# Kernel optimization log

Measured on AMD Instinct MI355X. Metric: run time of the kernel, lower is better.

The kernel has to match this reference:

```python
import jax, jax.numpy as jnp
import numpy as np

D = 1024   # visual_dim
N = 64     # num_phrases(1) * topN(64)
DEG = 16   # edges per subject row (incl. one guaranteed via a permutation)
E = N * DEG
T = 2      # cfg.MODEL.RELATION.VISUAL_GRAPH_PASSING_TIME


def _graph():
    rng = np.random.default_rng(0)
    perm = rng.permutation(N)
    mask = np.zeros((N, N), bool)
    for i in range(N):
        mask[i, perm[i]] = True  # permutation guarantees every column is covered
        pool = np.delete(np.arange(N), perm[i])
        mask[i, rng.choice(pool, DEG - 1, replace=False)] = True
    hdim, wdim = np.nonzero(mask)  # row-major, exactly E entries
    conn = np.full((N, N), -1, np.int32)
    conn[hdim, wdim] = np.arange(hdim.shape[0])
    edge_idx = hdim * N + wdim  # original: hdim*topN + wdim (topN == N since num_phrases == 1)
    return conn, edge_idx.astype(np.int32)


def setup_inputs():
    conn, edge_idx = _graph()
    key = jax.random.key(0)
    ks = jax.random.split(key, 16)
    p = lambda k, shp: jax.random.normal(k, shp, jnp.float32) * 0.02
    return {
        'visual_feat': jax.random.normal(ks[0], (N, D), jnp.float32),
        'rel_visual_feat': jax.random.normal(ks[1], (E, D), jnp.float32),
        'conn_map': jnp.asarray(conn),
        'topN_boxes_ids': jnp.arange(N, dtype=jnp.int32)[None, :],  # only shape is used
        'edge_idx': jnp.asarray(edge_idx),
        'W_sub': p(ks[2], (D, D)),
        'W_obj': p(ks[3], (D, D)),
        'W_r2s': p(ks[4], (D, D)),
        'W_r2o': p(ks[5], (D, D)),
        'W_joint': p(ks[6], (D, 4 * D)),
        'W_ctx': p(ks[7], (D, 3 * D)),
        'W_rel_update': p(ks[8], (D, 3 * D)),
        'W_rel_joint': p(ks[9], (D, 4 * D)),
        'W_rel_ctx': p(ks[10], (D, 2 * D)),
        'W_node': p(ks[11], (D, 2 * D)),
        'b_node': jnp.zeros((D,), jnp.float32),
        'W_factor': p(ks[12], (D, 2 * D)),
    }


def _forward(visual_feat, rel_visual_feat, conn_map, edge_idx,
             W_sub, W_obj, W_r2s, W_r2o, W_joint, W_ctx, W_rel_update,
             W_rel_joint, W_rel_ctx, W_node, b_node, W_factor):
    n, d = visual_feat.shape
    scale = jnp.asarray(d, visual_feat.dtype) ** 0.5
    connected = conn_map >= 0
    # scatter edge features into the dense [N, N, D] grid
    rel_temp = (jnp.zeros((n * n, d), visual_feat.dtype)
                .at[edge_idx].set(rel_visual_feat)
                .reshape(n, n, d))
    rel_ctx = rel_temp
    vctx = visual_feat
    for _ in range(T):
        # joint node embedding  [N, D]
        vj = jnp.concatenate([visual_feat, vctx, visual_feat * vctx, vctx - visual_feat], 1) @ W_joint.T
        # joint edge embedding  [N, N, D] (1x1 conv == per-position linear)
        rj = jnp.einsum('ijd,od->ijo',
                        jnp.concatenate([rel_temp, rel_ctx, rel_temp * rel_ctx, rel_temp - rel_ctx], 2),
                        W_rel_joint)
        # node -> edge: cat(sub_tile, obj_tile, rj) @ W_rel_update, done without tiling
        Ws, Wo, Wr = W_rel_update[:, :d], W_rel_update[:, d:2 * d], W_rel_update[:, 2 * d:]
        rel_j = (vj @ Ws.T)[:, None, :] + (vj @ Wo.T)[None, :, :] + jnp.einsum('ijd,od->ijo', rj, Wr)
        # edge -> node attention scores (elementwise product of 1x1-conv outputs, summed over channels)
        s_sbj = jnp.einsum('id,ijd->ij', vj @ W_sub.T, jnp.einsum('ijd,od->ijo', rel_j, W_r2s)) / scale
        s_obj = jnp.einsum('jd,ijd->ij', vj @ W_obj.T, jnp.einsum('ijd,od->ijo', rel_j, W_r2o)) / scale
        w_sbj = jax.nn.softmax(jnp.where(connected, s_sbj, -jnp.inf), axis=1)
        w_obj = jax.nn.softmax(jnp.where(connected, s_obj, -jnp.inf), axis=0)
        ctx = jnp.concatenate([jnp.einsum('ijd,ij->id', rel_j, w_sbj),
                               jnp.einsum('ijd,ij->jd', rel_j, w_obj)], 1)
        vctx = jnp.concatenate([vctx, ctx], 1) @ W_ctx.T
        rel_ctx = jnp.einsum('ijd,od->ijo', jnp.concatenate([rel_ctx, rel_j], 2), W_rel_ctx)
    # gather back the valid edges and produce outputs
    rel_out = jnp.concatenate([rel_visual_feat, rel_ctx.reshape(-1, d)[edge_idx]], 1) @ W_factor.T
    v_out = jnp.concatenate([visual_feat, vctx], 1) @ W_node.T + b_node
    deg = connected.sum(1) + connected.sum(0)
    v_out = jnp.where((deg == 0)[:, None], visual_feat, v_out)  # isolated nodes pass through
    return rel_out, v_out


def reference(visual_feat, rel_visual_feat, conn_map, topN_boxes_ids, edge_idx,
              W_sub, W_obj, W_r2s, W_r2o, W_joint, W_ctx, W_rel_update,
              W_rel_joint, W_rel_ctx, W_node, b_node, W_factor):
    del topN_boxes_ids  # only its shape is used in the original
    return _forward(visual_feat, rel_visual_feat, conn_map, edge_idx,
                    W_sub, W_obj, W_r2s, W_r2o, W_joint, W_ctx, W_rel_update,
                    W_rel_joint, W_rel_ctx, W_node, b_node, W_factor)
```

## Files before the change

kernel.cpp:

```cpp
#include <hip/hip_runtime.h>

static constexpr int kN = 64;
static constexpr int kD = 1024;
static constexpr int kE = 1024;
static constexpr int kT = 2;

typedef short  bf16x8 __attribute__((ext_vector_type(8)));
typedef float  f32x4  __attribute__((ext_vector_type(4)));
typedef unsigned short us8 __attribute__((ext_vector_type(8)));
typedef unsigned short us4 __attribute__((ext_vector_type(4)));

__device__ __forceinline__ unsigned short f2b(float f) {
    unsigned int u = __builtin_bit_cast(unsigned int, f);
    u += 0x7FFFu + ((u >> 16) & 1u);
    return (unsigned short)(u >> 16);
}
__device__ __forceinline__ float b2f(unsigned short u) {
    unsigned int x = ((unsigned int)u) << 16;
    return __builtin_bit_cast(float, x);
}
__device__ __forceinline__ bf16x8 cvt8(float4 a, float4 b) {
    us8 o;
    o[0] = f2b(a.x); o[1] = f2b(a.y); o[2] = f2b(a.z); o[3] = f2b(a.w);
    o[4] = f2b(b.x); o[5] = f2b(b.y); o[6] = f2b(b.z); o[7] = f2b(b.w);
    return __builtin_bit_cast(bf16x8, o);
}

struct ASrc { const unsigned short* s0; const unsigned short* s1; const unsigned short* s2; int mode; };

__device__ __forceinline__ bf16x8 loadA8(const ASrc& s, int row, int kg) {
    const int seg = kg >> 10, k = kg & 1023;
    const size_t ro = (size_t)row * 1024 + k;
    if (s.mode == 1) {
        const unsigned short* p = (seg == 0) ? s.s0 : (seg == 1 ? s.s1 : s.s2);
        return *(const bf16x8*)(p + ro);
    }
    const bf16x8 a = *(const bf16x8*)(s.s0 + ro);
    if (seg == 0) return a;
    const bf16x8 b = *(const bf16x8*)(s.s1 + ro);
    const us8 ua = __builtin_bit_cast(us8, a), ub = __builtin_bit_cast(us8, b);
    us8 o;
#pragma unroll
    for (int q = 0; q < 8; ++q) o[q] = f2b(b2f(ua[q]) * b2f(ub[q]));
    return __builtin_bit_cast(bf16x8, o);
}

struct GJob { ASrc a; const unsigned short* W; int ldw; void* P; int M; int K; int KS; int pbf; };
struct GJobs { GJob j[5]; int t0[6]; int nj; };

__global__ __launch_bounds__(256)
void k_gemm(GJobs G)
{
    __shared__ unsigned short lds[12288];
    const int flat = blockIdx.x;
    int ji = 0;
    while (ji + 1 < G.nj && flat >= G.t0[ji + 1]) ++ji;
    const GJob J = G.j[ji];
    const int local = flat - G.t0[ji];
    const int rowTiles = J.M >> 6;
    const int rt = local & (rowTiles - 1);
    const int rest = local / rowTiles;
    const int ct = rest & 7, z = rest >> 3;
    const int rowBase = rt * 64, colBase = ct * 128;
    const int kchunk = J.K / J.KS, kbeg = z * kchunk, kend = kbeg + kchunk;

    const int tid = threadIdx.x, lane = tid & 63, wid = tid >> 6;
    const int sr = tid >> 3, sc8 = tid & 7;
    const int wc8 = (sc8 ^ (sr & 7)) * 8;

    bf16x8 ra[2], rb[4];
    auto stage = [&](int kt) {
#pragma unroll
        for (int h = 0; h < 2; ++h)
            ra[h] = loadA8(J.a, rowBase + sr + 32 * h, kt + sc8 * 8);
#pragma unroll
        for (int h = 0; h < 4; ++h)
            rb[h] = *(const bf16x8*)(J.W + (size_t)(colBase + sr + 32 * h) * J.ldw + kt + sc8 * 8);
    };

    f32x4 acc[2][4] = {};
    const int wr = wid >> 1, wc = wid & 1;
    const int l15 = lane & 15, l4 = lane >> 4;

    stage(kbeg);
    for (int kt = kbeg; kt < kend; kt += 64) {
        __syncthreads();
#pragma unroll
        for (int h = 0; h < 2; ++h)
            *(bf16x8*)&lds[(sr + 32 * h) * 64 + wc8] = ra[h];
#pragma unroll
        for (int h = 0; h < 4; ++h)
            *(bf16x8*)&lds[4096 + (sr + 32 * h) * 64 + wc8] = rb[h];
        __syncthreads();
        if (kt + 64 < kend) stage(kt + 64);
#pragma unroll
        for (int kk = 0; kk < 2; ++kk) {
            const int c8 = kk * 4 + l4;
            bf16x8 af[2], bv[4];
#pragma unroll
            for (int m = 0; m < 2; ++m) {
                const int ar = wr * 32 + m * 16 + l15;
                af[m] = *(const bf16x8*)&lds[ar * 64 + (c8 ^ (ar & 7)) * 8];
            }
#pragma unroll
            for (int n = 0; n < 4; ++n) {
                const int br = wc * 64 + n * 16 + l15;
                bv[n] = *(const bf16x8*)&lds[4096 + br * 64 + (c8 ^ (br & 7)) * 8];
            }
#pragma unroll
            for (int m = 0; m < 2; ++m)
#pragma unroll
                for (int n = 0; n < 4; ++n)
                    acc[m][n] = __builtin_amdgcn_mfma_f32_16x16x32_bf16(af[m], bv[n], acc[m][n], 0, 0, 0);
        }
    }

    if (J.pbf) {
        __syncthreads();
#pragma unroll
        for (int m = 0; m < 2; ++m)
#pragma unroll
            for (int n = 0; n < 4; ++n)
#pragma unroll
                for (int r = 0; r < 4; ++r)
                    lds[(wr * 32 + m * 16 + l4 * 4 + r) * 132 + wc * 64 + n * 16 + l15] =
                        f2b(acc[m][n][r]);
        __syncthreads();
        unsigned short* Pb = (unsigned short*)J.P + (size_t)z * J.M * 1024;
#pragma unroll
        for (int c = tid; c < 1024; c += 256) {
            const int row = c >> 4, ch = c & 15;
            *(bf16x8*)(Pb + (size_t)(rowBase + row) * 1024 + colBase + ch * 8) =
                *(const bf16x8*)&lds[row * 132 + ch * 8];
        }
    } else {
        float* base = (float*)J.P + (size_t)z * J.M * 1024;
#pragma unroll
        for (int m = 0; m < 2; ++m) {
            const int row = rowBase + wr * 32 + m * 16 + l4 * 4;
#pragma unroll
            for (int n = 0; n < 4; ++n) {
                const int col = colBase + wc * 64 + n * 16 + l15;
#pragma unroll
                for (int r = 0; r < 4; ++r)
                    base[(size_t)(row + r) * 1024 + col] = acc[m][n][r];
            }
        }
    }
}

struct RJob { const void* P; int MO8; int KS; int pbf; float* Cf; unsigned short* Cb;
              const unsigned short* addb; const float* bias; int gather; };
struct RJobs { RJob j[6]; int t0[7]; int nj; const int* eidx; const float* gP; int gKS; };

__global__ void k_reduce(RJobs R)
{
    const int flat = blockIdx.x;
    int ji = 0;
    while (ji + 1 < R.nj && flat >= R.t0[ji + 1]) ++ji;
    const RJob J = R.j[ji];
    const int i8 = (flat - R.t0[ji]) * 256 + threadIdx.x;
    if (i8 >= J.MO8) return;
    float s[8] = {0.f, 0.f, 0.f, 0.f, 0.f, 0.f, 0.f, 0.f};
    if (J.pbf) {
        const unsigned short* P = (const unsigned short*)J.P;
        for (int z = 0; z < J.KS; ++z) {
            const us8 v = *(const us8*)(P + (size_t)z * J.MO8 * 8 + (size_t)i8 * 8);
#pragma unroll
            for (int q = 0; q < 8; ++q) s[q] += b2f(v[q]);
        }
    } else {
        const float* P = (const float*)J.P;
        for (int z = 0; z < J.KS; ++z) {
            const float* p = P + (size_t)z * J.MO8 * 8 + (size_t)i8 * 8;
            const float4 v0 = *(const float4*)p;
            const float4 v1 = *(const float4*)(p + 4);
            s[0] += v0.x; s[1] += v0.y; s[2] += v0.z; s[3] += v0.w;
            s[4] += v1.x; s[5] += v1.y; s[6] += v1.z; s[7] += v1.w;
        }
    }
    if (J.addb) {
        const us8 v = *(const us8*)(J.addb + (size_t)i8 * 8);
#pragma unroll
        for (int q = 0; q < 8; ++q) s[q] += b2f(v[q]);
    }
    if (J.gather) {
        const int e = i8 >> 7, c8 = i8 & 127;
        const int idx = R.eidx[e];
        const float* as_ = R.gP + (size_t)(idx >> 6) * 1024 + c8 * 8;
        const float* ao_ = R.gP + 131072 + (size_t)(idx & 63) * 1024 + c8 * 8;
        for (int z = 0; z < R.gKS; ++z) {
#pragma unroll
            for (int q = 0; q < 8; ++q)
                s[q] += as_[(size_t)z * 65536 + q] + ao_[(size_t)z * 65536 + q];
        }
    }
    if (J.bias) {
        const int c8 = i8 & 127;
#pragma unroll
        for (int q = 0; q < 8; ++q) s[q] += J.bias[c8 * 8 + q];
    }
    if (J.Cf) {
        *(float4*)(J.Cf + (size_t)i8 * 8)     = make_float4(s[0], s[1], s[2], s[3]);
        *(float4*)(J.Cf + (size_t)i8 * 8 + 4) = make_float4(s[4], s[5], s[6], s[7]);
    }
    if (J.Cb) {
        us8 o;
#pragma unroll
        for (int q = 0; q < 8; ++q) o[q] = f2b(s[q]);
        *(us8*)(J.Cb + (size_t)i8 * 8) = o;
    }
}

struct ConvBatch { const float* s[7]; unsigned short* d[7]; int beg8[7]; int total8; };
__global__ void k_f2b_batch(ConvBatch cb)
{
    int i = blockIdx.x * blockDim.x + threadIdx.x;
    if (i >= cb.total8) return;
    int k = 0;
    while (k < 6 && i >= cb.beg8[k + 1]) ++k;
    const int j = i - cb.beg8[k];
    const float4 v0 = reinterpret_cast<const float4*>(cb.s[k])[2 * j];
    const float4 v1 = reinterpret_cast<const float4*>(cb.s[k])[2 * j + 1];
    const bf16x8 o = cvt8(v0, v1);
    *(bf16x8*)(cb.d[k] + (size_t)j * 8) = o;
}

struct T4 { const float* s[4]; unsigned short* d[4]; };
__global__ __launch_bounds__(256)
void k_transpose(T4 t4)
{
    __shared__ float tile[64][65];
    const float* __restrict__ src = t4.s[blockIdx.z];
    unsigned short* __restrict__ dst = t4.d[blockIdx.z];
    const int bx = blockIdx.x * 64, by = blockIdx.y * 64;
    const int c = threadIdx.x & 63, r0 = threadIdx.x >> 6;
#pragma unroll
    for (int h = 0; h < 16; ++h) {
        const int r = r0 * 16 + h;
        tile[r][c] = src[(size_t)(by + r) * 1024 + bx + c];
    }
    __syncthreads();
#pragma unroll
    for (int h = 0; h < 16; ++h) {
        const int kk = r0 * 16 + h;
        dst[(size_t)(bx + kk) * 1024 + by + c] = f2b(tile[c][kk]);
    }
}

__global__ __launch_bounds__(256)
void k_buildW(const float* __restrict__ Wrel, const float* __restrict__ Wjnt,
              unsigned short* __restrict__ WrtRel, unsigned short* __restrict__ WeffRel,
              unsigned short* __restrict__ UrtVj, unsigned short* __restrict__ UeffVj)
{
    const int idx = blockIdx.x * 256 + threadIdx.x;
    const int o = idx >> 8, j = (idx & 255) * 4;
    const float* W = blockIdx.z ? Wjnt : Wrel;
    const float sgn = blockIdx.z ? -1.f : 1.f;
    unsigned short* rt = blockIdx.z ? UrtVj : WrtRel;
    unsigned short* ef = blockIdx.z ? UeffVj : WeffRel;
    const float4 w1 = *(const float4*)(W + (size_t)o * 4096 + j);
    const float4 w2 = *(const float4*)(W + (size_t)o * 4096 + 1024 + j);
    const float4 w3 = *(const float4*)(W + (size_t)o * 4096 + 2048 + j);
    const float4 w4 = *(const float4*)(W + (size_t)o * 4096 + 3072 + j);
    us4 t;
    t.x = f2b(w1.x + sgn * w4.x); t.y = f2b(w1.y + sgn * w4.y);
    t.z = f2b(w1.z + sgn * w4.z); t.w = f2b(w1.w + sgn * w4.w);
    *(us4*)(rt + (size_t)o * 1024 + j) = t;
    t.x = f2b(w2.x - sgn * w4.x); t.y = f2b(w2.y - sgn * w4.y);
    t.z = f2b(w2.z - sgn * w4.z); t.w = f2b(w2.w - sgn * w4.w);
    *(us4*)(ef + (size_t)o * 2048 + j) = t;
    t.x = f2b(w3.x); t.y = f2b(w3.y); t.z = f2b(w3.z); t.w = f2b(w3.w);
    *(us4*)(ef + (size_t)o * 2048 + 1024 + j) = t;
}

__global__ __launch_bounds__(256)
void k_scores(const float* __restrict__ qws, const float* __restrict__ qwo,
              const float* __restrict__ relj, const int* __restrict__ eidx,
              float* __restrict__ s_sbj, float* __restrict__ s_obj)
{
    const int e = blockIdx.x, t = threadIdx.x;
    const int idx = eidx[e];
    const int i = idx >> 6, j = idx & 63;
    const float4 r = reinterpret_cast<const float4*>(relj)[(size_t)e * 256 + t];
    const float4 a = reinterpret_cast<const float4*>(qws)[(size_t)i * 256 + t];
    const float4 b = reinterpret_cast<const float4*>(qwo)[(size_t)j * 256 + t];
    float vs = a.x * r.x + a.y * r.y + a.z * r.z + a.w * r.w;
    float vo = b.x * r.x + b.y * r.y + b.z * r.z + b.w * r.w;
    for (int off = 32; off; off >>= 1) {
        vs += __shfl_down(vs, off);
        vo += __shfl_down(vo, off);
    }
    __shared__ float ss[4], so[4];
    const int w = t >> 6, lane = t & 63;
    if (lane == 0) { ss[w] = vs; so[w] = vo; }
    __syncthreads();
    if (t == 0) {
        s_sbj[e] = (ss[0] + ss[1] + ss[2] + ss[3]) * 0.03125f;
        s_obj[e] = (so[0] + so[1] + so[2] + so[3]) * 0.03125f;
    }
}

__global__ __launch_bounds__(256)
void k_ctx12(const float* __restrict__ relj, const float* __restrict__ s_sbj,
             const float* __restrict__ s_obj, const int* __restrict__ conn,
             unsigned short* __restrict__ ctx1b, unsigned short* __restrict__ ctx2b)
{
    const int bid = blockIdx.x, t = threadIdx.x;
    const float4* relj4 = reinterpret_cast<const float4*>(relj);
    float4 acc = make_float4(0.f, 0.f, 0.f, 0.f);
    if (bid < 64) {
        const int i = bid;
        float sv[16];
        float m = -1e30f;
#pragma unroll
        for (int q = 0; q < 16; ++q) { sv[q] = s_sbj[i * 16 + q]; m = fmaxf(m, sv[q]); }
        float sum = 0.f;
#pragma unroll
        for (int q = 0; q < 16; ++q) { sv[q] = expf(sv[q] - m); sum += sv[q]; }
        const float inv = 1.f / sum;
#pragma unroll
        for (int q = 0; q < 16; ++q) {
            const float w = sv[q] * inv;
            const float4 v = relj4[(size_t)(i * 16 + q) * 256 + t];
            acc.x += w * v.x; acc.y += w * v.y; acc.z += w * v.z; acc.w += w * v.w;
        }
        us4 o; o.x = f2b(acc.x); o.y = f2b(acc.y); o.z = f2b(acc.z); o.w = f2b(acc.w);
        *(us4*)(ctx1b + (size_t)bid * 1024 + t * 4) = o;
    } else {
        const int j = bid - 64;
        __shared__ float sl[64];
        __shared__ int el[64];
        if (t < 64) {
            const int e = conn[t * kN + j];
            el[t] = e;
            sl[t] = (e >= 0) ? s_obj[e] : -1e30f;
        }
        __syncthreads();
        float m = -1e30f;
        for (int i = 0; i < 64; ++i) m = fmaxf(m, sl[i]);
        __syncthreads();
        if (t < 64) sl[t] = (el[t] >= 0) ? expf(sl[t] - m) : 0.f;
        __syncthreads();
        float sum = 0.f;
        for (int i = 0; i < 64; ++i) sum += sl[i];
        const float inv = 1.f / sum;
        for (int i = 0; i < 64; ++i) {
            const int e = el[i];
            if (e >= 0) {
                const float w = sl[i] * inv;
                const float4 v = relj4[(size_t)e * 256 + t];
                acc.x += w * v.x; acc.y += w * v.y; acc.z += w * v.z; acc.w += w * v.w;
            }
        }
        us4 o; o.x = f2b(acc.x); o.y = f2b(acc.y); o.z = f2b(acc.z); o.w = f2b(acc.w);
        *(us4*)(ctx2b + (size_t)j * 1024 + t * 4) = o;
    }
}

extern "C" void kernel_launch(void* const* d_in, const int* in_sizes, int n_in,
                              void* d_out, int out_size, void* d_ws, size_t ws_size,
                              hipStream_t stream)
{
    const float* visual   = (const float*)d_in[0];
    const float* relvis   = (const float*)d_in[1];
    const int*   conn     = (const int*)d_in[2];
    const int*   edge_idx = (const int*)d_in[4];
    const float* W_sub    = (const float*)d_in[5];
    const float* W_obj    = (const float*)d_in[6];
    const float* W_r2s    = (const float*)d_in[7];
    const float* W_r2o    = (const float*)d_in[8];
    const float* W_joint  = (const float*)d_in[9];
    const float* W_ctx    = (const float*)d_in[10];
    const float* W_relu   = (const float*)d_in[11];
    const float* W_relj   = (const float*)d_in[12];
    const float* W_relc   = (const float*)d_in[13];
    const float* W_node   = (const float*)d_in[14];
    const float* b_node   = (const float*)d_in[15];
    const float* W_factor = (const float*)d_in[16];
    (void)in_sizes; (void)n_in; (void)out_size; (void)ws_size;

    float* ws = (float*)d_ws;
    size_t off = 0;
    auto allocF = [&](size_t n) { float* p = ws + off; off += n; return p; };
    auto allocU = [&](size_t n) { return (unsigned short*)allocF((n + 1) / 2); };

    float* partF = allocF((size_t)1024 * 1024);
    unsigned short* partB = allocU((size_t)16 * 1024 * 1024);
    float* asqw  = allocF((size_t)4 * 64 * 1024);
    float* relj  = allocF((size_t)kE * kD);
    float* s_sbj = allocF(kE);
    float* s_obj = allocF(kE);
    unsigned short* relvis_b = allocU((size_t)kE * kD);
    unsigned short* visual_b = allocU((size_t)kN * kD);
    unsigned short* vj_b   = allocU((size_t)kN * kD);
    unsigned short* rj_b   = allocU((size_t)kE * kD);
    unsigned short* relj_b = allocU((size_t)kE * kD);
    unsigned short* rc_bA  = allocU((size_t)kE * kD);
    unsigned short* rc_bB  = allocU((size_t)kE * kD);
    unsigned short* vctx_bA = allocU((size_t)kN * kD);
    unsigned short* vctx_bB = allocU((size_t)kN * kD);
    unsigned short* ctx1_b = allocU((size_t)kN * kD);
    unsigned short* ctx2_b = allocU((size_t)kN * kD);
    unsigned short* R0_b = allocU((size_t)kE * kD);
    unsigned short* G0_b = allocU((size_t)kN * kD);
    unsigned short* Wb_ctx    = allocU((size_t)kD * 3 * kD);
    unsigned short* Wb_relu   = allocU((size_t)kD * 3 * kD);
    unsigned short* Wb_relc   = allocU((size_t)kD * 2 * kD);
    unsigned short* Wb_node   = allocU((size_t)kD * 2 * kD);
    unsigned short* Wb_factor = allocU((size_t)kD * 2 * kD);
    unsigned short* WsubT = allocU((size_t)kD * kD);
    unsigned short* WobjT = allocU((size_t)kD * kD);
    unsigned short* Wr2sT = allocU((size_t)kD * kD);
    unsigned short* Wr2oT = allocU((size_t)kD * kD);
    unsigned short* Wc_s  = allocU((size_t)kD * kD);
    unsigned short* Wc_o  = allocU((size_t)kD * kD);
    unsigned short* WrtRel  = allocU((size_t)kD * kD);
    unsigned short* WeffRel = allocU((size_t)kD * 2 * kD);
    unsigned short* UrtVj   = allocU((size_t)kD * kD);
    unsigned short* UeffVj  = allocU((size_t)kD * 2 * kD);

    auto seg1 = [](const unsigned short* a) {
        ASrc s; s.s0 = a; s.s1 = nullptr; s.s2 = nullptr; s.mode = 1; return s;
    };
    auto seg2 = [](const unsigned short* a, const unsigned short* b) {
        ASrc s; s.s0 = a; s.s1 = b; s.s2 = nullptr; s.mode = 1; return s;
    };
    auto seg3 = [](const unsigned short* a, const unsigned short* b, const unsigned short* c) {
        ASrc s; s.s0 = a; s.s1 = b; s.s2 = c; s.mode = 1; return s;
    };
    auto prodA = [](const unsigned short* c, const unsigned short* x) {
        ASrc s; s.s0 = c; s.s1 = x; s.s2 = nullptr; s.mode = 2; return s;
    };

    GJobs G; RJobs R;
    int gn = 0, gt = 0, rn = 0, rtt = 0;
    auto gAdd = [&](ASrc a, const unsigned short* W, int ldw, void* P, int M, int K, int KS, int pbf) {
        G.j[gn].a = a; G.j[gn].W = W; G.j[gn].ldw = ldw; G.j[gn].P = P;
        G.j[gn].M = M; G.j[gn].K = K; G.j[gn].KS = KS; G.j[gn].pbf = pbf;
        G.t0[gn] = gt; gt += KS * (M >> 6) * 8; ++gn;
    };
    auto gLaunch = [&]() {
        G.nj = gn; G.t0[gn] = gt;
        hipLaunchKernelGGL(k_gemm, dim3(gt), dim3(256), 0, stream, G);
        gn = 0; gt = 0;
    };
    auto rAdd = [&](const void* P, int MO8, int KS, int pbf, float* Cf, unsigned short* Cb,
                    const unsigned short* addb, const float* bias, int gather) {
        R.j[rn].P = P; R.j[rn].MO8 = MO8; R.j[rn].KS = KS; R.j[rn].pbf = pbf;
        R.j[rn].Cf = Cf; R.j[rn].Cb = Cb; R.j[rn].addb = addb; R.j[rn].bias = bias;
        R.j[rn].gather = gather;
        R.t0[rn] = rtt; rtt += (MO8 + 255) / 256; ++rn;
    };
    auto rLaunch = [&](const int* eidx, const float* gP, int gKS) {
        R.nj = rn; R.t0[rn] = rtt; R.eidx = eidx; R.gP = gP; R.gKS = gKS;
        hipLaunchKernelGGL(k_reduce, dim3(rtt), dim3(256), 0, stream, R);
        rn = 0; rtt = 0;
    };

    {
        ConvBatch cb;
        const float* srcs[7] = {W_ctx, W_relu, W_relc, W_node, W_factor, relvis, visual};
        unsigned short* dsts[7] = {Wb_ctx, Wb_relu, Wb_relc, Wb_node, Wb_factor, relvis_b, visual_b};
        const int nel[7] = {3 * 1024 * 1024, 3 * 1024 * 1024, 2 * 1024 * 1024,
                            2 * 1024 * 1024, 2 * 1024 * 1024, 1024 * 1024, 64 * 1024};
        int cum = 0;
        for (int k = 0; k < 7; ++k) { cb.s[k] = srcs[k]; cb.d[k] = dsts[k]; cb.beg8[k] = cum; cum += nel[k] / 8; }
        cb.total8 = cum;
        hipLaunchKernelGGL(k_f2b_batch, dim3((cum + 255) / 256), dim3(256), 0, stream, cb);
    }
    {
        T4 t4;
        t4.s[0] = W_sub; t4.d[0] = WsubT;
        t4.s[1] = W_obj; t4.d[1] = WobjT;
        t4.s[2] = W_r2s; t4.d[2] = Wr2sT;
        t4.s[3] = W_r2o; t4.d[3] = Wr2oT;
        hipLaunchKernelGGL(k_transpose, dim3(16, 16, 4), dim3(256), 0, stream, t4);
    }
    hipLaunchKernelGGL(k_buildW, dim3(1024, 1, 2), dim3(256), 0, stream,
                       W_relj, W_joint, WrtRel, WeffRel, UrtVj, UeffVj);

    const size_t PB1 = (size_t)4 * 1024 * 1024;
    gAdd(seg1(Wr2sT), WsubT, 1024, partB, 1024, 1024, 4, 1);
    gAdd(seg1(Wr2oT), WobjT, 1024, partB + PB1, 1024, 1024, 4, 1);
    gAdd(seg1(relvis_b), WrtRel, 1024, partB + 2 * PB1, 1024, 1024, 4, 1);
    gAdd(seg1(visual_b), UrtVj, 1024, partF, 64, 1024, 4, 0);
    gLaunch();
    rAdd(partB, 131072, 4, 1, nullptr, Wc_s, nullptr, nullptr, 0);
    rAdd(partB + PB1, 131072, 4, 1, nullptr, Wc_o, nullptr, nullptr, 0);
    rAdd(partB + 2 * PB1, 131072, 4, 1, nullptr, R0_b, nullptr, nullptr, 0);
    rAdd(partF, 8192, 4, 0, nullptr, G0_b, nullptr, nullptr, 0);
    rLaunch(nullptr, nullptr, 0);

    for (int t = 0; t < kT; ++t) {
        const unsigned short* vcur  = (t == 0) ? visual_b : vctx_bA;
        unsigned short*       vnext = (t == 0) ? vctx_bA : vctx_bB;
        const unsigned short* rccur = (t == 0) ? relvis_b : rc_bA;
        unsigned short*       rcnext = (t == 0) ? rc_bA : rc_bB;

        gAdd(prodA(vcur, visual_b), UeffVj, 2048, partF, 64, 2048, 8, 0);
        gAdd(prodA(rccur, relvis_b), WeffRel, 2048, partB, 1024, 2048, 8, 1);
        gLaunch();
        rAdd(partF, 8192, 8, 0, nullptr, vj_b, G0_b, nullptr, 0);
        rAdd(partB, 131072, 8, 1, nullptr, rj_b, R0_b, nullptr, 0);
        rLaunch(nullptr, nullptr, 0);

        gAdd(seg1(vj_b), Wb_relu,        3072, partF,          64, 1024, 2, 0);
        gAdd(seg1(vj_b), Wb_relu + 1024, 3072, partF + 131072, 64, 1024, 2, 0);
        gAdd(seg1(vj_b), Wc_s,           1024, partF + 262144, 64, 1024, 2, 0);
        gAdd(seg1(vj_b), Wc_o,           1024, partF + 393216, 64, 1024, 2, 0);
        gAdd(seg1(rj_b), Wb_relu + 2048, 3072, partB,        1024, 1024, 4, 1);
        gLaunch();
        rAdd(partF,          8192, 2, 0, asqw,          nullptr, nullptr, nullptr, 0);
        rAdd(partF + 131072, 8192, 2, 0, asqw + 65536,  nullptr, nullptr, nullptr, 0);
        rAdd(partF + 262144, 8192, 2, 0, asqw + 131072, nullptr, nullptr, nullptr, 0);
        rAdd(partF + 393216, 8192, 2, 0, asqw + 196608, nullptr, nullptr, nullptr, 0);
        rAdd(partB, 131072, 4, 1, relj, relj_b, nullptr, nullptr, 1);
        rLaunch(edge_idx, partF, 2);

        hipLaunchKernelGGL(k_scores, dim3(kE), dim3(256), 0, stream,
                           asqw + 131072, asqw + 196608, relj, edge_idx, s_sbj, s_obj);
        hipLaunchKernelGGL(k_ctx12, dim3(128), dim3(256), 0, stream,
                           relj, s_sbj, s_obj, conn, ctx1_b, ctx2_b);

        gAdd(seg3(vcur, ctx1_b, ctx2_b), Wb_ctx, 3072, partF, 64, 3072, 8, 0);
        gAdd(seg2(rccur, relj_b), Wb_relc, 2048, partB, 1024, 2048, 8, 1);
        gLaunch();
        rAdd(partF, 8192, 8, 0, nullptr, vnext, nullptr, nullptr, 0);
        rAdd(partB, 131072, 8, 1, nullptr, rcnext, nullptr, nullptr, 0);
        rLaunch(nullptr, nullptr, 0);
    }

    float* rel_out = (float*)d_out;
    float* v_out   = (float*)d_out + (size_t)kE * kD;
    gAdd(seg2(relvis_b, rc_bB), Wb_factor, 2048, partB, 1024, 2048, 4, 1);
    gAdd(seg2(visual_b, vctx_bB), Wb_node, 2048, partF, 64, 2048, 8, 0);
    gLaunch();
    rAdd(partB, 131072, 4, 1, rel_out, nullptr, nullptr, nullptr, 0);
    rAdd(partF, 8192, 8, 0, v_out, nullptr, nullptr, b_node, 0);
    rLaunch(nullptr, nullptr, 0);
}
```

Baseline: 222.4 us.

## Use 128-row GEMM tiles with register-resident B and fuse score into context kernel

For large-M GEMM jobs the kernel now uses 128x128 tiles and a 4x4 MFMA accumulator per wave. B fragments are loaded straight from global memory into registers with double buffering, and only A is staged through LDS. This cuts LDS traffic and the block count, and raises per-wave compute density, at the cost of higher register pressure and fewer blocks for parallelism. Separately, the per-edge score kernel is folded into the context softmax kernel, which computes the dot products itself and removes one launch plus the score round-trip through global memory.

```diff
diff --git a/kernel.cpp b/kernel.cpp
--- a/kernel.cpp
+++ b/kernel.cpp
@@ -51,93 +51,153 @@
 __global__ __launch_bounds__(256)
 void k_gemm(GJobs G)
 {
-    __shared__ unsigned short lds[12288];
+    __shared__ unsigned short lds[16896];
     const int flat = blockIdx.x;
     int ji = 0;
     while (ji + 1 < G.nj && flat >= G.t0[ji + 1]) ++ji;
     const GJob J = G.j[ji];
     const int local = flat - G.t0[ji];
-    const int rowTiles = J.M >> 6;
-    const int rt = local & (rowTiles - 1);
-    const int rest = local / rowTiles;
-    const int ct = rest & 7, z = rest >> 3;
-    const int rowBase = rt * 64, colBase = ct * 128;
-    const int kchunk = J.K / J.KS, kbeg = z * kchunk, kend = kbeg + kchunk;
-
     const int tid = threadIdx.x, lane = tid & 63, wid = tid >> 6;
+    const int l15 = lane & 15, l4 = lane >> 4;
     const int sr = tid >> 3, sc8 = tid & 7;
     const int wc8 = (sc8 ^ (sr & 7)) * 8;
 
-    bf16x8 ra[2], rb[4];
-    auto stage = [&](int kt) {
-#pragma unroll
-        for (int h = 0; h < 2; ++h)
-            ra[h] = loadA8(J.a, rowBase + sr + 32 * h, kt + sc8 * 8);
-#pragma unroll
-        for (int h = 0; h < 4; ++h)
-            rb[h] = *(const bf16x8*)(J.W + (size_t)(colBase + sr + 32 * h) * J.ldw + kt + sc8 * 8);
-    };
-
-    f32x4 acc[2][4] = {};
-    const int wr = wid >> 1, wc = wid & 1;
-    const int l15 = lane & 15, l4 = lane >> 4;
-
-    stage(kbeg);
-    for (int kt = kbeg; kt < kend; kt += 64) {
+    if (J.M >= 128) {
+        const int rowTiles = J.M >> 7;
+        const int rt = local % rowTiles;
+        const int rest = local / rowTiles;
+        const int ct = rest & 7, z = rest >> 3;
+        const int rowBase = rt * 128, colBase = ct * 128;
+        const int kchunk = J.K / J.KS, kbeg = z * kchunk, kend = kbeg + kchunk;
+        const int wr = wid >> 1, wc = wid & 1;
+
+        f32x4 acc[4][4] = {};
+        bf16x8 ra[4], rb0[8], rb1[8];
+        const unsigned short* Bbase =
+            J.W + (size_t)(colBase + wc * 64 + l15) * J.ldw + l4 * 8;
+
+        auto stageA = [&](int kt) {
+#pragma unroll
+            for (int h = 0; h < 4; ++h)
+                ra[h] = loadA8(J.a, rowBase + sr + 32 * h, kt + sc8 * 8);
+        };
+        auto loadB = [&](int kt, bf16x8* rb) {
+#pragma unroll
+            for (int n = 0; n < 4; ++n) {
+                rb[n]     = *(const bf16x8*)(Bbase + (size_t)(n * 16) * J.ldw + kt);
+                rb[4 + n] = *(const bf16x8*)(Bbase + (size_t)(n * 16) * J.ldw + kt + 32);
+            }
+        };
+        auto writeA = [&]() {
+#pragma unroll
+            for (int h = 0; h < 4; ++h)
+                *(bf16x8*)&lds[(sr + 32 * h) * 64 + wc8] = ra[h];
+        };
+        auto compute = [&](bf16x8* rb) {
+#pragma unroll
+            for (int kk = 0; kk < 2; ++kk) {
+                bf16x8 af[4];
+#pragma unroll
+                for (int m = 0; m < 4; ++m) {
+                    const int ar = wr * 64 + m * 16 + l15;
+                    af[m] = *(const bf16x8*)&lds[ar * 64 + (((kk << 2) | l4) ^ (ar & 7)) * 8];
+                }
+#pragma unroll
+                for (int m = 0; m < 4; ++m)
+#pragma unroll
+                    for (int n = 0; n < 4; ++n)
+                        acc[m][n] = __builtin_amdgcn_mfma_f32_16x16x32_bf16(
+                            af[m], rb[kk * 4 + n], acc[m][n], 0, 0, 0);
+            }
+        };
+
+        stageA(kbeg); loadB(kbeg, rb0);
+        for (int kt = kbeg; kt < kend; kt += 128) {
+            __syncthreads();
+            writeA();
+            __syncthreads();
+            const bool more1 = (kt + 64 < kend);
+            if (more1) { stageA(kt + 64); loadB(kt + 64, rb1); }
+            compute(rb0);
+            if (!more1) break;
+            __syncthreads();
+            writeA();
+            __syncthreads();
+            const bool more2 = (kt + 128 < kend);
+            if (more2) { stageA(kt + 128); loadB(kt + 128, rb0); }
+            compute(rb1);
+        }
+
         __syncthreads();
 #pragma unroll
-        for (int h = 0; h < 2; ++h)
-            *(bf16x8*)&lds[(sr + 32 * h) * 64 + wc8] = ra[h];
-#pragma unroll
-        for (int h = 0; h < 4; ++h)
-            *(bf16x8*)&lds[4096 + (sr + 32 * h) * 64 + wc8] = rb[h];
-        __syncthreads();
-        if (kt + 64 < kend) stage(kt + 64);
-#pragma unroll
-        for (int kk = 0; kk < 2; ++kk) {
-            const int c8 = kk * 4 + l4;
-            bf16x8 af[2], bv[4];
-#pragma unroll
-            for (int m = 0; m < 2; ++m) {
-                const int ar = wr * 32 + m * 16 + l15;
-                af[m] = *(const bf16x8*)&lds[ar * 64 + (c8 ^ (ar & 7)) * 8];
-            }
-#pragma unroll
-            for (int n = 0; n < 4; ++n) {
-                const int br = wc * 64 + n * 16 + l15;
-                bv[n] = *(const bf16x8*)&lds[4096 + br * 64 + (c8 ^ (br & 7)) * 8];
-            }
-#pragma unroll
-            for (int m = 0; m < 2; ++m)
-#pragma unroll
-                for (int n = 0; n < 4; ++n)
-                    acc[m][n] = __builtin_amdgcn_mfma_f32_16x16x32_bf16(af[m], bv[n], acc[m][n], 0, 0, 0);
-        }
-    }
-
-    if (J.pbf) {
-        __syncthreads();
-#pragma unroll
-        for (int m = 0; m < 2; ++m)
+        for (int m = 0; m < 4; ++m)
 #pragma unroll
             for (int n = 0; n < 4; ++n)
 #pragma unroll
                 for (int r = 0; r < 4; ++r)
-                    lds[(wr * 32 + m * 16 + l4 * 4 + r) * 132 + wc * 64 + n * 16 + l15] =
+                    lds[(wr * 64 + m * 16 + l4 * 4 + r) * 132 + wc * 64 + n * 16 + l15] =
                         f2b(acc[m][n][r]);
         __syncthreads();
         unsigned short* Pb = (unsigned short*)J.P + (size_t)z * J.M * 1024;
 #pragma unroll
-        for (int c = tid; c < 1024; c += 256) {
+        for (int c = tid; c < 2048; c += 256) {
             const int row = c >> 4, ch = c & 15;
             *(bf16x8*)(Pb + (size_t)(rowBase + row) * 1024 + colBase + ch * 8) =
                 *(const bf16x8*)&lds[row * 132 + ch * 8];
         }
     } else {
+        const int ct = local & 7, z = local >> 3;
+        const int colBase = ct * 128;
+        const int kchunk = J.K / J.KS, kbeg = z * kchunk, kend = kbeg + kchunk;
+        const int wr = wid >> 1, wc = wid & 1;
+
+        bf16x8 ra[2], rb[4];
+        auto stage = [&](int kt) {
+#pragma unroll
+            for (int h = 0; h < 2; ++h)
+                ra[h] = loadA8(J.a, sr + 32 * h, kt + sc8 * 8);
+#pragma unroll
+            for (int h = 0; h < 4; ++h)
+                rb[h] = *(const bf16x8*)(J.W + (size_t)(colBase + sr + 32 * h) * J.ldw + kt + sc8 * 8);
+        };
+
+        f32x4 acc[2][4] = {};
+        stage(kbeg);
+        for (int kt = kbeg; kt < kend; kt += 64) {
+            __syncthreads();
+#pragma unroll
+            for (int h = 0; h < 2; ++h)
+                *(bf16x8*)&lds[(sr + 32 * h) * 64 + wc8] = ra[h];
+#pragma unroll
+            for (int h = 0; h < 4; ++h)
+                *(bf16x8*)&lds[4096 + (sr + 32 * h) * 64 + wc8] = rb[h];
+            __syncthreads();
+            if (kt + 64 < kend) stage(kt + 64);
+#pragma unroll
+            for (int kk = 0; kk < 2; ++kk) {
+                const int c8 = kk * 4 + l4;
+                bf16x8 af[2], bv[4];
+#pragma unroll
+                for (int m = 0; m < 2; ++m) {
+                    const int ar = wr * 32 + m * 16 + l15;
+                    af[m] = *(const bf16x8*)&lds[ar * 64 + (c8 ^ (ar & 7)) * 8];
+                }
+#pragma unroll
+                for (int n = 0; n < 4; ++n) {
+                    const int br = wc * 64 + n * 16 + l15;
+                    bv[n] = *(const bf16x8*)&lds[4096 + br * 64 + (c8 ^ (br & 7)) * 8];
+                }
+#pragma unroll
+                for (int m = 0; m < 2; ++m)
+#pragma unroll
+                    for (int n = 0; n < 4; ++n)
+                        acc[m][n] = __builtin_amdgcn_mfma_f32_16x16x32_bf16(af[m], bv[n], acc[m][n], 0, 0, 0);
+            }
+        }
         float* base = (float*)J.P + (size_t)z * J.M * 1024;
 #pragma unroll
         for (int m = 0; m < 2; ++m) {
-            const int row = rowBase + wr * 32 + m * 16 + l4 * 4;
+            const int row = wr * 32 + m * 16 + l4 * 4;
 #pragma unroll
             for (int n = 0; n < 4; ++n) {
                 const int col = colBase + wc * 64 + n * 16 + l15;
@@ -275,46 +335,40 @@
 }
 
 __global__ __launch_bounds__(256)
-void k_scores(const float* __restrict__ qws, const float* __restrict__ qwo,
-              const float* __restrict__ relj, const int* __restrict__ eidx,
-              float* __restrict__ s_sbj, float* __restrict__ s_obj)
-{
-    const int e = blockIdx.x, t = threadIdx.x;
-    const int idx = eidx[e];
-    const int i = idx >> 6, j = idx & 63;
-    const float4 r = reinterpret_cast<const float4*>(relj)[(size_t)e * 256 + t];
-    const float4 a = reinterpret_cast<const float4*>(qws)[(size_t)i * 256 + t];
-    const float4 b = reinterpret_cast<const float4*>(qwo)[(size_t)j * 256 + t];
-    float vs = a.x * r.x + a.y * r.y + a.z * r.z + a.w * r.w;
-    float vo = b.x * r.x + b.y * r.y + b.z * r.z + b.w * r.w;
-    for (int off = 32; off; off >>= 1) {
-        vs += __shfl_down(vs, off);
-        vo += __shfl_down(vo, off);
-    }
-    __shared__ float ss[4], so[4];
-    const int w = t >> 6, lane = t & 63;
-    if (lane == 0) { ss[w] = vs; so[w] = vo; }
-    __syncthreads();
-    if (t == 0) {
-        s_sbj[e] = (ss[0] + ss[1] + ss[2] + ss[3]) * 0.03125f;
-        s_obj[e] = (so[0] + so[1] + so[2] + so[3]) * 0.03125f;
-    }
-}
-
-__global__ __launch_bounds__(256)
-void k_ctx12(const float* __restrict__ relj, const float* __restrict__ s_sbj,
-             const float* __restrict__ s_obj, const int* __restrict__ conn,
-             unsigned short* __restrict__ ctx1b, unsigned short* __restrict__ ctx2b)
+void k_sctx(const float* __restrict__ relj, const float* __restrict__ qws,
+            const float* __restrict__ qwo, const int* __restrict__ conn,
+            unsigned short* __restrict__ ctx1b, unsigned short* __restrict__ ctx2b)
 {
     const int bid = blockIdx.x, t = threadIdx.x;
     const float4* relj4 = reinterpret_cast<const float4*>(relj);
+    __shared__ float sl[64];
+    __shared__ int el[64];
     float4 acc = make_float4(0.f, 0.f, 0.f, 0.f);
+
     if (bid < 64) {
         const int i = bid;
+        {
+            const int g = t >> 4, l = t & 15;
+            const size_t e4 = (size_t)(i * 16 + g) * 256;
+            const float4* q4 = reinterpret_cast<const float4*>(qws) + (size_t)i * 256;
+            float v = 0.f;
+#pragma unroll
+            for (int q = 0; q < 16; ++q) {
+                const float4 r = relj4[e4 + l + q * 16];
+                const float4 a = q4[l + q * 16];
+                v += a.x * r.x + a.y * r.y + a.z * r.z + a.w * r.w;
+            }
+            v += __shfl_xor(v, 1, 16);
+            v += __shfl_xor(v, 2, 16);
+            v += __shfl_xor(v, 4, 16);
+            v += __shfl_xor(v, 8, 16);
+            if (l == 0) sl[g] = v * 0.03125f;
+        }
+        __syncthreads();
         float sv[16];
         float m = -1e30f;
 #pragma unroll
-        for (int q = 0; q < 16; ++q) { sv[q] = s_sbj[i * 16 + q]; m = fmaxf(m, sv[q]); }
+        for (int q = 0; q < 16; ++q) { sv[q] = sl[q]; m = fmaxf(m, sv[q]); }
         float sum = 0.f;
 #pragma unroll
         for (int q = 0; q < 16; ++q) { sv[q] = expf(sv[q] - m); sum += sv[q]; }
@@ -326,29 +380,42 @@
             acc.x += w * v.x; acc.y += w * v.y; acc.z += w * v.z; acc.w += w * v.w;
         }
         us4 o; o.x = f2b(acc.x); o.y = f2b(acc.y); o.z = f2b(acc.z); o.w = f2b(acc.w);
-        *(us4*)(ctx1b + (size_t)bid * 1024 + t * 4) = o;
+        *(us4*)(ctx1b + (size_t)i * 1024 + t * 4) = o;
     } else {
         const int j = bid - 64;
-        __shared__ float sl[64];
-        __shared__ int el[64];
-        if (t < 64) {
-            const int e = conn[t * kN + j];
-            el[t] = e;
-            sl[t] = (e >= 0) ? s_obj[e] : -1e30f;
+        {
+            const int i = t >> 2, sub = t & 3;
+            const int e = conn[i * kN + j];
+            if (sub == 0) el[i] = e;
+            float v = 0.f;
+            if (e >= 0) {
+                const size_t e4 = (size_t)e * 256;
+                const float4* q4 = reinterpret_cast<const float4*>(qwo) + (size_t)j * 256;
+#pragma unroll
+                for (int q = 0; q < 64; ++q) {
+                    const float4 r = relj4[e4 + sub + q * 4];
+                    const float4 a = q4[sub + q * 4];
+                    v += a.x * r.x + a.y * r.y + a.z * r.z + a.w * r.w;
+                }
+            }
+            v += __shfl_xor(v, 1, 4);
+            v += __shfl_xor(v, 2, 4);
+            if (sub == 0) sl[i] = (e >= 0) ? v * 0.03125f : -1e30f;
         }
         __syncthreads();
         float m = -1e30f;
         for (int i = 0; i < 64; ++i) m = fmaxf(m, sl[i]);
-        __syncthreads();
-        if (t < 64) sl[t] = (el[t] >= 0) ? expf(sl[t] - m) : 0.f;
-        __syncthreads();
         float sum = 0.f;
-        for (int i = 0; i < 64; ++i) sum += sl[i];
+        float ex[64];
+        for (int i = 0; i < 64; ++i) {
+            ex[i] = (el[i] >= 0) ? expf(sl[i] - m) : 0.f;
+            sum += ex[i];
+        }
         const float inv = 1.f / sum;
         for (int i = 0; i < 64; ++i) {
             const int e = el[i];
             if (e >= 0) {
-                const float w = sl[i] * inv;
+                const float w = ex[i] * inv;
                 const float4 v = relj4[(size_t)e * 256 + t];
                 acc.x += w * v.x; acc.y += w * v.y; acc.z += w * v.z; acc.w += w * v.w;
             }
@@ -389,8 +456,6 @@
     unsigned short* partB = allocU((size_t)16 * 1024 * 1024);
     float* asqw  = allocF((size_t)4 * 64 * 1024);
     float* relj  = allocF((size_t)kE * kD);
-    float* s_sbj = allocF(kE);
-    float* s_obj = allocF(kE);
     unsigned short* relvis_b = allocU((size_t)kE * kD);
     unsigned short* visual_b = allocU((size_t)kN * kD);
     unsigned short* vj_b   = allocU((size_t)kN * kD);
@@ -438,7 +503,9 @@
     auto gAdd = [&](ASrc a, const unsigned short* W, int ldw, void* P, int M, int K, int KS, int pbf) {
         G.j[gn].a = a; G.j[gn].W = W; G.j[gn].ldw = ldw; G.j[gn].P = P;
         G.j[gn].M = M; G.j[gn].K = K; G.j[gn].KS = KS; G.j[gn].pbf = pbf;
-        G.t0[gn] = gt; gt += KS * (M >> 6) * 8; ++gn;
+        G.t0[gn] = gt;
+        gt += (M >= 128) ? KS * (M >> 7) * 8 : KS * 8;
+        ++gn;
     };
     auto gLaunch = [&]() {
         G.nj = gn; G.t0[gn] = gt;
@@ -518,10 +585,8 @@
         rAdd(partB, 131072, 4, 1, relj, relj_b, nullptr, nullptr, 1);
         rLaunch(edge_idx, partF, 2);
 
-        hipLaunchKernelGGL(k_scores, dim3(kE), dim3(256), 0, stream,
-                           asqw + 131072, asqw + 196608, relj, edge_idx, s_sbj, s_obj);
-        hipLaunchKernelGGL(k_ctx12, dim3(128), dim3(256), 0, stream,
-                           relj, s_sbj, s_obj, conn, ctx1_b, ctx2_b);
+        hipLaunchKernelGGL(k_sctx, dim3(128), dim3(256), 0, stream,
+                           relj, asqw + 131072, asqw + 196608, conn, ctx1_b, ctx2_b);
 
         gAdd(seg3(vcur, ctx1_b, ctx2_b), Wb_ctx, 3072, partF, 64, 3072, 8, 0);
         gAdd(seg2(rccur, relj_b), Wb_relc, 2048, partB, 1024, 2048, 8, 1);
```

Result: slower. 278.6 us (+25.3%).

## Merge precompute GEMMs into first iteration's batched launch and fold reductions

Applied to the files above, without the earlier changes.

The separate precompute GEMM launch and its reduce launch are removed. Those four GEMMs are now added to the first iteration's joint GEMM batch, and their split-K partials (R0, G0) are summed directly inside the joint reduce through a second partial-source field, so the bf16 R0/G0 intermediates are never materialized. This removes two kernel launches and their serialization gaps and gives the first batched launch more blocks. In exchange, the reduce now reads more partial data per job (fp32/bf16 partials instead of one bf16 tensor), and the first iteration re-reads R0p/G0p partials in the second iteration too.

```diff
diff --git a/kernel.cpp b/kernel.cpp
--- a/kernel.cpp
+++ b/kernel.cpp
@@ -46,7 +46,7 @@
 }
 
 struct GJob { ASrc a; const unsigned short* W; int ldw; void* P; int M; int K; int KS; int pbf; };
-struct GJobs { GJob j[5]; int t0[6]; int nj; };
+struct GJobs { GJob j[6]; int t0[7]; int nj; };
 
 __global__ __launch_bounds__(256)
 void k_gemm(GJobs G)
@@ -65,8 +65,10 @@
     const int kchunk = J.K / J.KS, kbeg = z * kchunk, kend = kbeg + kchunk;
 
     const int tid = threadIdx.x, lane = tid & 63, wid = tid >> 6;
+    const int l15 = lane & 15, l4 = lane >> 4;
     const int sr = tid >> 3, sc8 = tid & 7;
     const int wc8 = (sc8 ^ (sr & 7)) * 8;
+    const int wr = wid >> 1, wc = wid & 1;
 
     bf16x8 ra[2], rb[4];
     auto stage = [&](int kt) {
@@ -79,9 +81,6 @@
     };
 
     f32x4 acc[2][4] = {};
-    const int wr = wid >> 1, wc = wid & 1;
-    const int l15 = lane & 15, l4 = lane >> 4;
-
     stage(kbeg);
     for (int kt = kbeg; kt < kend; kt += 64) {
         __syncthreads();
@@ -149,7 +148,9 @@
     }
 }
 
-struct RJob { const void* P; int MO8; int KS; int pbf; float* Cf; unsigned short* Cb;
+struct RJob { const void* P; int MO8; int KS; int pbf;
+              const void* P2; int KS2; int pbf2;
+              float* Cf; unsigned short* Cb;
               const unsigned short* addb; const float* bias; int gather; };
 struct RJobs { RJob j[6]; int t0[7]; int nj; const int* eidx; const float* gP; int gKS; };
 
@@ -177,6 +178,25 @@
             const float4 v1 = *(const float4*)(p + 4);
             s[0] += v0.x; s[1] += v0.y; s[2] += v0.z; s[3] += v0.w;
             s[4] += v1.x; s[5] += v1.y; s[6] += v1.z; s[7] += v1.w;
+        }
+    }
+    if (J.P2) {
+        if (J.pbf2) {
+            const unsigned short* P = (const unsigned short*)J.P2;
+            for (int z = 0; z < J.KS2; ++z) {
+                const us8 v = *(const us8*)(P + (size_t)z * J.MO8 * 8 + (size_t)i8 * 8);
+#pragma unroll
+                for (int q = 0; q < 8; ++q) s[q] += b2f(v[q]);
+            }
+        } else {
+            const float* P = (const float*)J.P2;
+            for (int z = 0; z < J.KS2; ++z) {
+                const float* p = P + (size_t)z * J.MO8 * 8 + (size_t)i8 * 8;
+                const float4 v0 = *(const float4*)p;
+                const float4 v1 = *(const float4*)(p + 4);
+                s[0] += v0.x; s[1] += v0.y; s[2] += v0.z; s[3] += v0.w;
+                s[4] += v1.x; s[5] += v1.y; s[6] += v1.z; s[7] += v1.w;
+            }
         }
     }
     if (J.addb) {
@@ -387,6 +407,8 @@
 
     float* partF = allocF((size_t)1024 * 1024);
     unsigned short* partB = allocU((size_t)16 * 1024 * 1024);
+    float* G0p  = allocF((size_t)4 * 65536);
+    unsigned short* R0p = allocU((size_t)4 * 1024 * 1024);
     float* asqw  = allocF((size_t)4 * 64 * 1024);
     float* relj  = allocF((size_t)kE * kD);
     float* s_sbj = allocF(kE);
@@ -402,8 +424,6 @@
     unsigned short* vctx_bB = allocU((size_t)kN * kD);
     unsigned short* ctx1_b = allocU((size_t)kN * kD);
     unsigned short* ctx2_b = allocU((size_t)kN * kD);
-    unsigned short* R0_b = allocU((size_t)kE * kD);
-    unsigned short* G0_b = allocU((size_t)kN * kD);
     unsigned short* Wb_ctx    = allocU((size_t)kD * 3 * kD);
     unsigned short* Wb_relu   = allocU((size_t)kD * 3 * kD);
     unsigned short* Wb_relc   = allocU((size_t)kD * 2 * kD);
@@ -445,9 +465,12 @@
         hipLaunchKernelGGL(k_gemm, dim3(gt), dim3(256), 0, stream, G);
         gn = 0; gt = 0;
     };
-    auto rAdd = [&](const void* P, int MO8, int KS, int pbf, float* Cf, unsigned short* Cb,
+    auto rAdd = [&](const void* P, int MO8, int KS, int pbf,
+                    const void* P2, int KS2, int pbf2,
+                    float* Cf, unsigned short* Cb,
                     const unsigned short* addb, const float* bias, int gather) {
         R.j[rn].P = P; R.j[rn].MO8 = MO8; R.j[rn].KS = KS; R.j[rn].pbf = pbf;
+        R.j[rn].P2 = P2; R.j[rn].KS2 = KS2; R.j[rn].pbf2 = pbf2;
         R.j[rn].Cf = Cf; R.j[rn].Cb = Cb; R.j[rn].addb = addb; R.j[rn].bias = bias;
         R.j[rn].gather = gather;
         R.t0[rn] = rtt; rtt += (MO8 + 255) / 256; ++rn;
@@ -480,17 +503,8 @@
     hipLaunchKernelGGL(k_buildW, dim3(1024, 1, 2), dim3(256), 0, stream,
                        W_relj, W_joint, WrtRel, WeffRel, UrtVj, UeffVj);
 
-    const size_t PB1 = (size_t)4 * 1024 * 1024;
-    gAdd(seg1(Wr2sT), WsubT, 1024, partB, 1024, 1024, 4, 1);
-    gAdd(seg1(Wr2oT), WobjT, 1024, partB + PB1, 1024, 1024, 4, 1);
-    gAdd(seg1(relvis_b), WrtRel, 1024, partB + 2 * PB1, 1024, 1024, 4, 1);
-    gAdd(seg1(visual_b), UrtVj, 1024, partF, 64, 1024, 4, 0);
-    gLaunch();
-    rAdd(partB, 131072, 4, 1, nullptr, Wc_s, nullptr, nullptr, 0);
-    rAdd(partB + PB1, 131072, 4, 1, nullptr, Wc_o, nullptr, nullptr, 0);
-    rAdd(partB + 2 * PB1, 131072, 4, 1, nullptr, R0_b, nullptr, nullptr, 0);
-    rAdd(partF, 8192, 4, 0, nullptr, G0_b, nullptr, nullptr, 0);
-    rLaunch(nullptr, nullptr, 0);
+    const size_t M8 = (size_t)8 * 1024 * 1024;
+    const size_t M12 = (size_t)12 * 1024 * 1024;
 
     for (int t = 0; t < kT; ++t) {
         const unsigned short* vcur  = (t == 0) ? visual_b : vctx_bA;
@@ -500,9 +514,19 @@
 
         gAdd(prodA(vcur, visual_b), UeffVj, 2048, partF, 64, 2048, 8, 0);
         gAdd(prodA(rccur, relvis_b), WeffRel, 2048, partB, 1024, 2048, 8, 1);
+        if (t == 0) {
+            gAdd(seg1(Wr2sT), WsubT, 1024, partB + M8,  1024, 1024, 4, 1);
+            gAdd(seg1(Wr2oT), WobjT, 1024, partB + M12, 1024, 1024, 4, 1);
+            gAdd(seg1(relvis_b), WrtRel, 1024, R0p, 1024, 1024, 4, 1);
+            gAdd(seg1(visual_b), UrtVj, 1024, G0p, 64, 1024, 4, 0);
+        }
         gLaunch();
-        rAdd(partF, 8192, 8, 0, nullptr, vj_b, G0_b, nullptr, 0);
-        rAdd(partB, 131072, 8, 1, nullptr, rj_b, R0_b, nullptr, 0);
+        rAdd(partF, 8192, 8, 0, G0p, 4, 0, nullptr, vj_b, nullptr, nullptr, 0);
+        rAdd(partB, 131072, 8, 1, R0p, 4, 1, nullptr, rj_b, nullptr, nullptr, 0);
+        if (t == 0) {
+            rAdd(partB + M8,  131072, 4, 1, nullptr, 0, 0, nullptr, Wc_s, nullptr, nullptr, 0);
+            rAdd(partB + M12, 131072, 4, 1, nullptr, 0, 0, nullptr, Wc_o, nullptr, nullptr, 0);
+        }
         rLaunch(nullptr, nullptr, 0);
 
         gAdd(seg1(vj_b), Wb_relu,        3072, partF,          64, 1024, 2, 0);
@@ -511,11 +535,11 @@
         gAdd(seg1(vj_b), Wc_o,           1024, partF + 393216, 64, 1024, 2, 0);
         gAdd(seg1(rj_b), Wb_relu + 2048, 3072, partB,        1024, 1024, 4, 1);
         gLaunch();
-        rAdd(partF,          8192, 2, 0, asqw,          nullptr, nullptr, nullptr, 0);
-        rAdd(partF + 131072, 8192, 2, 0, asqw + 65536,  nullptr, nullptr, nullptr, 0);
-        rAdd(partF + 262144, 8192, 2, 0, asqw + 131072, nullptr, nullptr, nullptr, 0);
-        rAdd(partF + 393216, 8192, 2, 0, asqw + 196608, nullptr, nullptr, nullptr, 0);
-        rAdd(partB, 131072, 4, 1, relj, relj_b, nullptr, nullptr, 1);
+        rAdd(partF,          8192, 2, 0, nullptr, 0, 0, asqw,          nullptr, nullptr, nullptr, 0);
+        rAdd(partF + 131072, 8192, 2, 0, nullptr, 0, 0, asqw + 65536,  nullptr, nullptr, nullptr, 0);
+        rAdd(partF + 262144, 8192, 2, 0, nullptr, 0, 0, asqw + 131072, nullptr, nullptr, nullptr, 0);
+        rAdd(partF + 393216, 8192, 2, 0, nullptr, 0, 0, asqw + 196608, nullptr, nullptr, nullptr, 0);
+        rAdd(partB, 131072, 4, 1, nullptr, 0, 0, relj, relj_b, nullptr, nullptr, 1);
         rLaunch(edge_idx, partF, 2);
 
         hipLaunchKernelGGL(k_scores, dim3(kE), dim3(256), 0, stream,
@@ -526,8 +550,8 @@
         gAdd(seg3(vcur, ctx1_b, ctx2_b), Wb_ctx, 3072, partF, 64, 3072, 8, 0);
         gAdd(seg2(rccur, relj_b), Wb_relc, 2048, partB, 1024, 2048, 8, 1);
         gLaunch();
-        rAdd(partF, 8192, 8, 0, nullptr, vnext, nullptr, nullptr, 0);
-        rAdd(partB, 131072, 8, 1, nullptr, rcnext, nullptr, nullptr, 0);
+        rAdd(partF, 8192, 8, 0, nullptr, 0, 0, nullptr, vnext, nullptr, nullptr, 0);
+        rAdd(partB, 131072, 8, 1, nullptr, 0, 0, nullptr, rcnext, nullptr, nullptr, 0);
         rLaunch(nullptr, nullptr, 0);
     }
 
@@ -536,7 +560,7 @@
     gAdd(seg2(relvis_b, rc_bB), Wb_factor, 2048, partB, 1024, 2048, 4, 1);
     gAdd(seg2(visual_b, vctx_bB), Wb_node, 2048, partF, 64, 2048, 8, 0);
     gLaunch();
-    rAdd(partB, 131072, 4, 1, rel_out, nullptr, nullptr, nullptr, 0);
-    rAdd(partF, 8192, 8, 0, v_out, nullptr, nullptr, b_node, 0);
+    rAdd(partB, 131072, 4, 1, nullptr, 0, 0, rel_out, nullptr, nullptr, nullptr, 0);
+    rAdd(partF, 8192, 8, 0, nullptr, 0, 0, v_out, nullptr, nullptr, b_node, 0);
     rLaunch(nullptr, nullptr, 0);
 }
```

Result: faster. 215.0 us (-3.3%).
